# Kernel optimization log

Hardware: AMD Instinct MI355X
Metric: run time of the kernel (lower is better)

## Reference

```python
import jax, jax.numpy as jnp
import numpy as np

B, T, DM, H, D = 2, 4096, 1024, 16, 64
HD = H * D
PHASE_SCALE = 10.0


def _multiscale_phasors(num_heads, head_dim):
    # Deterministic multiscale frequencies: RoPE-like geometric spacing over
    # the feature dim, with a per-head octave scale (reconstruction of the
    # registered buffer `freqs` from generate_multiscale_phasors).
    d = np.arange(head_dim, dtype=np.float32) / head_dim
    base = 10000.0 ** (-d)                      # (D,)
    head_scale = 2.0 ** (-np.arange(num_heads, dtype=np.float32))  # (H,)
    return jnp.asarray(2.0 * np.pi * head_scale[:, None] * base[None, :],
                       dtype=jnp.float32)       # (H, D)


def setup_inputs() -> dict:
    key = jax.random.key(0)
    k0, k1, k2, k3 = jax.random.split(key, 4)
    x = jax.random.normal(k0, (B, T, DM), jnp.float32)
    Wk = jax.random.normal(k1, (DM, HD), jnp.float32) / np.float32(np.sqrt(DM))
    Wv = jax.random.normal(k2, (DM, HD), jnp.float32) / np.float32(np.sqrt(DM))
    Wo = jax.random.normal(k3, (HD, DM), jnp.float32) / np.float32(np.sqrt(HD))
    gate = jnp.full((H, 2), 0.5, jnp.float32)
    freqs = _multiscale_phasors(H, D)
    return {"x": x, "Wk": Wk, "Wv": Wv, "Wo": Wo, "gate": gate, "freqs": freqs}


def _holo_fused_step(v, binder, probe):
    # (cumsum(v * binder, dim=1) * probe).real / sqrt(1..T)
    mem = jnp.cumsum(v * binder, axis=1)                     # (B,T,H,D) complex64
    t = v.shape[1]
    scale = jnp.sqrt(jnp.arange(1, t + 1, dtype=jnp.float32))[None, :, None, None]
    return jnp.real(mem * probe) / scale                     # (B,T,H,D) float32


def reference(x, Wk, Wv, Wo, gate, freqs):
    Bb, Tt, _ = x.shape
    k_real = (x @ Wk).reshape(Bb, Tt, H, D)                  # (B,T,H,D)
    v = (x @ Wv).reshape(Bb, Tt, H, D).astype(jnp.complex64)
    k = jnp.exp(1j * (k_real * PHASE_SCALE))                 # unit phasors, q = k
    # Positional path: rotors = exp(i * t * freqs)
    t = jnp.arange(Tt, dtype=jnp.float32)
    rotors = jnp.exp(1j * (t[:, None, None] * freqs))[None]  # (1,T,H,D)
    out_pos = _holo_fused_step(v, rotors, jnp.conj(rotors))
    # Associative path: bind with conj of shifted keys, retrieve with q=k
    k_shifted = jnp.roll(k, 1, axis=1).at[:, 0].set(0.0)
    out_assoc = _holo_fused_step(v, jnp.conj(k_shifted), k)
    g_pos = gate[:, 0][None, None, :, None]
    g_assoc = gate[:, 1][None, None, :, None]
    out = out_pos * g_pos + out_assoc * g_assoc              # (B,T,H,D)
    return out.reshape(Bb, Tt, HD) @ Wo                      # dropout p=0 -> identity
```

## Files before the change

kernel.cpp:

```cpp
#include <hip/hip_runtime.h>


#define B_ 2
#define T_ 4096
#define DM_ 1024
#define H_ 16
#define D_ 64
#define M_ (B_*T_)
#define PHASE_SCALE 10.0f

typedef _Float16 f16;
typedef unsigned int u32;
typedef __attribute__((ext_vector_type(8))) _Float16 f16x8;
typedef __attribute__((ext_vector_type(4))) _Float16 f16x4;
typedef __attribute__((ext_vector_type(4))) float f32x4;


__global__ void k_cvt_f32_f16(const float* __restrict__ src, f16* __restrict__ dst, int n) {
  int i = blockIdx.x * blockDim.x + threadIdx.x;
  int idx = i * 4;
  if (idx < n) {
    float4 v = *reinterpret_cast<const float4*>(src + idx);
    f16x4 o;
    o[0] = (f16)v.x; o[1] = (f16)v.y; o[2] = (f16)v.z; o[3] = (f16)v.w;
    *reinterpret_cast<f16x4*>(dst + idx) = o;
  }
}

__global__ void k_transpose_cvt(const float* __restrict__ src, f16* __restrict__ dst) {
  __shared__ float tile[32][33];
  int bx = blockIdx.x;
  int by = blockIdx.y;
  int tx = threadIdx.x;
  int ty = threadIdx.y;
  #pragma unroll
  for (int r = 0; r < 32; r += 8)
    tile[ty + r][tx] = src[(size_t)(by * 32 + ty + r) * 1024 + bx * 32 + tx];
  __syncthreads();
  #pragma unroll
  for (int r = 0; r < 32; r += 8)
    dst[(size_t)(bx * 32 + ty + r) * 1024 + by * 32 + tx] = (f16)tile[tx][ty + r];
}


__device__ __forceinline__ void gl2lds16(const void* g, void* l) {
  __builtin_amdgcn_global_load_lds((const __attribute__((address_space(1))) u32*)g,
                                   (__attribute__((address_space(3))) u32*)l, 16, 0, 0);
}

__launch_bounds__(256)
__global__ void k_gemm_f16(const f16* __restrict__ A, const f16* __restrict__ Bt,
                           float* __restrict__ C, int N, int K) {
  __shared__ f16 lA[128][32];
  __shared__ f16 lB[128][32];
  const int tid  = threadIdx.x;
  const int lane = tid & 63;
  const int wid  = tid >> 6;
  const int wr   = wid >> 1, wc = wid & 1;
  const int m0   = blockIdx.x * 128;
  const int n0   = blockIdx.y * 128;
  const int row_l = tid >> 2;
  const int seg   = (tid & 3) * 8;
  const int lr    = lane & 15;
  const int kofs  = (lane >> 4) * 8;

  f32x4 acc[4][4] = {};

  const f16* ga = A  + (size_t)(m0 + row_l) * K + seg;
  const f16* gb = Bt + (size_t)(n0 + row_l) * K + seg;

  for (int k0 = 0; k0 < K; k0 += 32) {
    gl2lds16(ga + k0,                 &lA[row_l][seg]);
    gl2lds16(ga + (size_t)64 * K + k0, &lA[64 + row_l][seg]);
    gl2lds16(gb + k0,                 &lB[row_l][seg]);
    gl2lds16(gb + (size_t)64 * K + k0, &lB[64 + row_l][seg]);
    __syncthreads();
    f16x8 af[4], bf[4];
    #pragma unroll
    for (int i = 0; i < 4; ++i)
      af[i] = *(const f16x8*)(&lA[wr * 64 + i * 16 + lr][kofs]);
    #pragma unroll
    for (int j = 0; j < 4; ++j)
      bf[j] = *(const f16x8*)(&lB[wc * 64 + j * 16 + lr][kofs]);
    #pragma unroll
    for (int i = 0; i < 4; ++i)
      #pragma unroll
      for (int j = 0; j < 4; ++j)
        acc[i][j] = __builtin_amdgcn_mfma_f32_16x16x32_f16(af[i], bf[j], acc[i][j], 0, 0, 0);
    __syncthreads();
  }

  const int rb = (lane >> 4) * 4;
  #pragma unroll
  for (int i = 0; i < 4; ++i) {
    const int row = m0 + wr * 64 + i * 16 + rb;
    #pragma unroll
    for (int j = 0; j < 4; ++j) {
      const int col = n0 + wc * 64 + j * 16 + lr;
      #pragma unroll
      for (int r = 0; r < 4; ++r)
        C[(size_t)(row + r) * N + col] = acc[i][j][r];
    }
  }
}


__global__ void k_scan_part(const float* __restrict__ kv, const float* __restrict__ freqs,
                            float4* __restrict__ tot) {
  const int bid = blockIdx.x;
  const int cg = bid & 15;
  const int h  = (bid >> 4) & 15;
  const int b  = bid >> 8;
  const int w  = threadIdx.x >> 6;
  const int d  = threadIdx.x & 63;
  const int c  = cg * 4 + w;
  const int t0 = c * 64;
  const int base = h * 64 + d;
  const float f = freqs[base];

  float bc = 0.f, bs = 0.f;
  if (t0 > 0) {
    float krp = kv[(size_t)(b * T_ + t0 - 1) * 2048 + base];
    float th = PHASE_SCALE * krp;
    bs = __sinf(th); bc = __cosf(th);
  }
  float pr = 0.f, pi = 0.f, ar = 0.f, ai = 0.f;
  #pragma unroll 4
  for (int tt = 0; tt < 64; ++tt) {
    int t = t0 + tt;
    size_t row = (size_t)(b * T_ + t) * 2048;
    float v  = kv[row + 1024 + base];
    float kr = kv[row + base];
    double rrev = (double)t * (double)f * 0.15915494309189535;
    rrev -= floor(rrev);
    float ph = (float)rrev * 6.28318530717958647692f;
    float sp = __sinf(ph), cp = __cosf(ph);
    pr += v * cp; pi += v * sp;
    ar += v * bc; ai -= v * bs;
    float th = PHASE_SCALE * kr;
    bs = __sinf(th); bc = __cosf(th);
  }
  tot[((size_t)(c * 2 + b) * 16 + h) * 64 + d] = make_float4(pr, pi, ar, ai);
}

__global__ void k_scan_carry(const float4* __restrict__ tot, float4* __restrict__ carry) {
  const int h = blockIdx.x & 15;
  const int b = blockIdx.x >> 4;
  const int d = threadIdx.x;
  float pr = 0.f, pi = 0.f, ar = 0.f, ai = 0.f;
  for (int c = 0; c < 64; ++c) {
    size_t idx = ((size_t)(c * 2 + b) * 16 + h) * 64 + d;
    float4 tv = tot[idx];
    carry[idx] = make_float4(pr, pi, ar, ai);
    pr += tv.x; pi += tv.y; ar += tv.z; ai += tv.w;
  }
}

__global__ void k_scan_out(const float* __restrict__ kv, const float* __restrict__ freqs,
                           const float4* __restrict__ carry, const float* __restrict__ gate,
                           f16* __restrict__ y) {
  const int bid = blockIdx.x;
  const int cg = bid & 15;
  const int h  = (bid >> 4) & 15;
  const int b  = bid >> 8;
  const int w  = threadIdx.x >> 6;
  const int d  = threadIdx.x & 63;
  const int c  = cg * 4 + w;
  const int t0 = c * 64;
  const int base = h * 64 + d;
  const float f = freqs[base];
  const float gp = gate[2 * h], ga = gate[2 * h + 1];

  float4 cr = carry[((size_t)(c * 2 + b) * 16 + h) * 64 + d];
  float pr = cr.x, pi = cr.y, ar = cr.z, ai = cr.w;
  float bc = 0.f, bs = 0.f;
  if (t0 > 0) {
    float krp = kv[(size_t)(b * T_ + t0 - 1) * 2048 + base];
    float th = PHASE_SCALE * krp;
    bs = __sinf(th); bc = __cosf(th);
  }
  #pragma unroll 4
  for (int tt = 0; tt < 64; ++tt) {
    int t = t0 + tt;
    size_t row = (size_t)(b * T_ + t) * 2048;
    float v  = kv[row + 1024 + base];
    float kr = kv[row + base];
    double rrev = (double)t * (double)f * 0.15915494309189535;
    rrev -= floor(rrev);
    float ph = (float)rrev * 6.28318530717958647692f;
    float sp = __sinf(ph), cp = __cosf(ph);
    pr += v * cp; pi += v * sp;
    ar += v * bc; ai -= v * bs;
    float th = PHASE_SCALE * kr;
    bs = __sinf(th); bc = __cosf(th);
    float inv = rsqrtf((float)(t + 1));
    float op = (pr * cp + pi * sp) * inv;
    float oa = (ar * bc - ai * bs) * inv;
    y[(size_t)(b * T_ + t) * 1024 + base] = (f16)(gp * op + ga * oa);
  }
}


extern "C" void kernel_launch(void* const* d_in, const int* in_sizes, int n_in,
                              void* d_out, int out_size, void* d_ws, size_t ws_size,
                              hipStream_t stream) {
  const float* x     = (const float*)d_in[0];
  const float* Wk    = (const float*)d_in[1];
  const float* Wv    = (const float*)d_in[2];
  const float* Wo    = (const float*)d_in[3];
  const float* gate  = (const float*)d_in[4];
  const float* freqs = (const float*)d_in[5];
  float* out = (float*)d_out;

  char* ws = (char*)d_ws;
  size_t off = 0;
  auto alloc = [&](size_t bytes) { void* p = ws + off; off += (bytes + 255) & ~255ull; return p; };

  f16*    xh    = (f16*)   alloc((size_t)M_ * DM_ * sizeof(f16));
  f16*    Wkvt  = (f16*)   alloc((size_t)2048 * 1024 * sizeof(f16));
  f16*    Wot   = (f16*)   alloc((size_t)1024 * 1024 * sizeof(f16));
  float*  kvb   = (float*) alloc((size_t)M_ * 2048 * sizeof(float));
  float4* tot   = (float4*)alloc((size_t)64 * B_ * H_ * D_ * sizeof(float4));
  float4* carry = (float4*)alloc((size_t)64 * B_ * H_ * D_ * sizeof(float4));
  f16*    yh    = xh;

  hipLaunchKernelGGL(k_cvt_f32_f16, dim3((M_ * DM_ / 4 + 255) / 256), dim3(256), 0, stream,
                     x, xh, M_ * DM_);
  hipLaunchKernelGGL(k_transpose_cvt, dim3(32, 32), dim3(32, 8), 0, stream, Wk, Wkvt);
  hipLaunchKernelGGL(k_transpose_cvt, dim3(32, 32), dim3(32, 8), 0, stream, Wv, Wkvt + (size_t)1024 * 1024);
  hipLaunchKernelGGL(k_transpose_cvt, dim3(32, 32), dim3(32, 8), 0, stream, Wo, Wot);
  hipLaunchKernelGGL(k_gemm_f16, dim3(64, 16), dim3(256), 0, stream, xh, Wkvt, kvb, 2048, 1024);
  hipLaunchKernelGGL(k_scan_part,  dim3(512), dim3(256), 0, stream, kvb, freqs, tot);
  hipLaunchKernelGGL(k_scan_carry, dim3(32),  dim3(64),  0, stream, tot, carry);
  hipLaunchKernelGGL(k_scan_out,   dim3(512), dim3(256), 0, stream, kvb, freqs, carry, gate, yh);
  hipLaunchKernelGGL(k_gemm_f16, dim3(64, 8), dim3(256), 0, stream, yh, Wot, out, 1024, 1024);
}
```

Before: 218.5 us.

## Replace GEMM with 256x256 pipelined swizzled kernel and restructure scan with rotor recurrence

```diff
diff --git a/kernel.cpp b/kernel.cpp
--- a/kernel.cpp
+++ b/kernel.cpp
@@ -3,7 +3,6 @@
 
 #define B_ 2
 #define T_ 4096
-#define DM_ 1024
 #define H_ 16
 #define D_ 64
 #define M_ (B_*T_)
@@ -17,8 +16,7 @@
 
 
 __global__ void k_cvt_f32_f16(const float* __restrict__ src, f16* __restrict__ dst, int n) {
-  int i = blockIdx.x * blockDim.x + threadIdx.x;
-  int idx = i * 4;
+  int idx = (blockIdx.x * blockDim.x + threadIdx.x) * 4;
   if (idx < n) {
     float4 v = *reinterpret_cast<const float4*>(src + idx);
     f16x4 o;
@@ -29,10 +27,8 @@
 
 __global__ void k_transpose_cvt(const float* __restrict__ src, f16* __restrict__ dst) {
   __shared__ float tile[32][33];
-  int bx = blockIdx.x;
-  int by = blockIdx.y;
-  int tx = threadIdx.x;
-  int ty = threadIdx.y;
+  int bx = blockIdx.x, by = blockIdx.y;
+  int tx = threadIdx.x, ty = threadIdx.y;
   #pragma unroll
   for (int r = 0; r < 32; r += 8)
     tile[ty + r][tx] = src[(size_t)(by * 32 + ty + r) * 1024 + bx * 32 + tx];
@@ -43,102 +39,174 @@
 }
 
 
-__device__ __forceinline__ void gl2lds16(const void* g, void* l) {
+__device__ __forceinline__ void gl2lds16(const f16* g, char* l) {
   __builtin_amdgcn_global_load_lds((const __attribute__((address_space(1))) u32*)g,
                                    (__attribute__((address_space(3))) u32*)l, 16, 0, 0);
 }
 
-__launch_bounds__(256)
-__global__ void k_gemm_f16(const f16* __restrict__ A, const f16* __restrict__ Bt,
-                           float* __restrict__ C, int N, int K) {
-  __shared__ f16 lA[128][32];
-  __shared__ f16 lB[128][32];
+#define S_BAR() __builtin_amdgcn_s_barrier()
+#define WAIT_LGKM0() do { asm volatile("s_waitcnt lgkmcnt(0)" ::: "memory"); \
+                          __builtin_amdgcn_sched_barrier(0); } while (0)
+#define WAIT_VM(n) asm volatile("s_waitcnt vmcnt(" #n ")" ::: "memory")
+
+#define STAGE(gp, ldsoff, kkt) do { \
+  gl2lds16((gp) + (size_t)(kkt) * 64,               smem + (ldsoff) + tid * 16); \
+  gl2lds16((gp) + (size_t)(kkt) * 64 + 64 * 1024,   smem + (ldsoff) + 8192 + tid * 16); \
+} while (0)
+
+#define PHASE(AH, BH, READ_A, VMW, STG) do { \
+  if (READ_A) { \
+    _Pragma("unroll") for (int mi = 0; mi < 4; ++mi) \
+    _Pragma("unroll") for (int kk = 0; kk < 2; ++kk) \
+      aF[mi][kk] = *(const f16x8*)(smem + curbuf + (AH) * 16384 + offA[mi][kk]); \
+  } \
+  _Pragma("unroll") for (int nj = 0; nj < 2; ++nj) \
+  _Pragma("unroll") for (int kk = 0; kk < 2; ++kk) \
+    bF[nj][kk] = *(const f16x8*)(smem + curbuf + 32768 + (BH) * 16384 + offB[nj][kk]); \
+  STG; \
+  S_BAR(); \
+  WAIT_LGKM0(); \
+  __builtin_amdgcn_s_setprio(1); \
+  _Pragma("unroll") for (int mi = 0; mi < 4; ++mi) \
+  _Pragma("unroll") for (int nj = 0; nj < 2; ++nj) \
+  _Pragma("unroll") for (int kk = 0; kk < 2; ++kk) \
+    acc[(AH) * 2 + (BH)][mi][nj] = __builtin_amdgcn_mfma_f32_16x16x32_f16( \
+        aF[mi][kk], bF[nj][kk], acc[(AH) * 2 + (BH)][mi][nj], 0, 0, 0); \
+  __builtin_amdgcn_s_setprio(0); \
+  VMW; \
+  S_BAR(); \
+} while (0)
+
+__launch_bounds__(512, 1)
+__global__ void k_gemm8(const f16* __restrict__ A, const f16* __restrict__ Bt,
+                        float* __restrict__ C32, f16* __restrict__ C16) {
+  extern __shared__ char smem[];
   const int tid  = threadIdx.x;
   const int lane = tid & 63;
   const int wid  = tid >> 6;
-  const int wr   = wid >> 1, wc = wid & 1;
-  const int m0   = blockIdx.x * 128;
-  const int n0   = blockIdx.y * 128;
-  const int row_l = tid >> 2;
-  const int seg   = (tid & 3) * 8;
-  const int lr    = lane & 15;
-  const int kofs  = (lane >> 4) * 8;
-
-  f32x4 acc[4][4] = {};
-
-  const f16* ga = A  + (size_t)(m0 + row_l) * K + seg;
-  const f16* gb = Bt + (size_t)(n0 + row_l) * K + seg;
-
-  for (int k0 = 0; k0 < K; k0 += 32) {
-    gl2lds16(ga + k0,                 &lA[row_l][seg]);
-    gl2lds16(ga + (size_t)64 * K + k0, &lA[64 + row_l][seg]);
-    gl2lds16(gb + k0,                 &lB[row_l][seg]);
-    gl2lds16(gb + (size_t)64 * K + k0, &lB[64 + row_l][seg]);
-    __syncthreads();
-    f16x8 af[4], bf[4];
+  const int wr   = wid >> 2, wc = wid & 3;
+  const int lr   = lane & 15, hi = lane >> 4;
+  const int m0   = blockIdx.x * 256;
+  const int n0   = blockIdx.y * 256;
+
+  const int rsub = tid >> 3;
+  const int csw  = ((tid & 7) ^ (rsub & 7)) * 8;
+  const f16* gA0 = A  + (size_t)(m0 + rsub) * 1024 + csw;
+  const f16* gA1 = gA0 + (size_t)128 * 1024;
+  const f16* gB0 = Bt + (size_t)(n0 + rsub) * 1024 + csw;
+  const f16* gB1 = gB0 + (size_t)128 * 1024;
+
+  int offA[4][2], offB[2][2];
+  #pragma unroll
+  for (int mi = 0; mi < 4; ++mi)
     #pragma unroll
-    for (int i = 0; i < 4; ++i)
-      af[i] = *(const f16x8*)(&lA[wr * 64 + i * 16 + lr][kofs]);
+    for (int kk = 0; kk < 2; ++kk) {
+      int row = wr * 64 + mi * 16 + lr;
+      offA[mi][kk] = row * 128 + (((kk * 4 + hi) ^ (row & 7)) << 4);
+    }
+  #pragma unroll
+  for (int nj = 0; nj < 2; ++nj)
     #pragma unroll
-    for (int j = 0; j < 4; ++j)
-      bf[j] = *(const f16x8*)(&lB[wc * 64 + j * 16 + lr][kofs]);
+    for (int kk = 0; kk < 2; ++kk) {
+      int row = wc * 32 + nj * 16 + lr;
+      offB[nj][kk] = row * 128 + (((kk * 4 + hi) ^ (row & 7)) << 4);
+    }
+
+  f32x4 acc[4][4][2] = {};
+  f16x8 aF[4][2], bF[2][2];
+
+  STAGE(gA0, 0,     0);
+  STAGE(gB0, 32768, 0);
+  STAGE(gA1, 16384, 0);
+  STAGE(gA0, 65536, 1);
+  STAGE(gB1, 49152, 0);
+  STAGE(gB0, 98304, 1);
+  WAIT_VM(8);
+  S_BAR();
+
+  for (int kt = 0; kt < 14; ++kt) {
+    const int curbuf = (kt & 1) * 65536;
+    const int nxtbuf = curbuf ^ 65536;
+    PHASE(0, 0, 1, WAIT_VM(4),  STAGE(gA1, nxtbuf + 16384, kt + 1));
+    PHASE(0, 1, 0, WAIT_VM(10), STAGE(gA0, curbuf + 0,     kt + 2));
+    PHASE(1, 0, 1, (void)0,     STAGE(gB1, nxtbuf + 49152, kt + 1));
+    PHASE(1, 1, 0, WAIT_VM(8),  STAGE(gB0, curbuf + 32768, kt + 2));
+  }
+  {
+    const int curbuf = 0, nxtbuf = 65536;
+    PHASE(0, 0, 1, WAIT_VM(4), STAGE(gA1, nxtbuf + 16384, 15));
+    PHASE(0, 1, 0, WAIT_VM(8), (void)0);
+    PHASE(1, 0, 1, (void)0,    STAGE(gB1, nxtbuf + 49152, 15));
+    PHASE(1, 1, 0, WAIT_VM(4), (void)0);
+  }
+  {
+    const int curbuf = 65536;
+    PHASE(0, 0, 1, WAIT_VM(0), (void)0);
+    PHASE(0, 1, 0, (void)0,    (void)0);
+    PHASE(1, 0, 1, (void)0,    (void)0);
+    PHASE(1, 1, 0, (void)0,    (void)0);
+  }
+
+  const int rb = hi * 4;
+  #pragma unroll
+  for (int ah = 0; ah < 2; ++ah)
     #pragma unroll
-    for (int i = 0; i < 4; ++i)
+    for (int bh = 0; bh < 2; ++bh)
       #pragma unroll
-      for (int j = 0; j < 4; ++j)
-        acc[i][j] = __builtin_amdgcn_mfma_f32_16x16x32_f16(af[i], bf[j], acc[i][j], 0, 0, 0);
-    __syncthreads();
-  }
-
-  const int rb = (lane >> 4) * 4;
-  #pragma unroll
-  for (int i = 0; i < 4; ++i) {
-    const int row = m0 + wr * 64 + i * 16 + rb;
-    #pragma unroll
-    for (int j = 0; j < 4; ++j) {
-      const int col = n0 + wc * 64 + j * 16 + lr;
-      #pragma unroll
-      for (int r = 0; r < 4; ++r)
-        C[(size_t)(row + r) * N + col] = acc[i][j][r];
-    }
-  }
-}
-
-
-__global__ void k_scan_part(const float* __restrict__ kv, const float* __restrict__ freqs,
-                            float4* __restrict__ tot) {
+      for (int mi = 0; mi < 4; ++mi)
+        #pragma unroll
+        for (int nj = 0; nj < 2; ++nj) {
+          f32x4 a4 = acc[ah * 2 + bh][mi][nj];
+          const int row = m0 + ah * 128 + wr * 64 + mi * 16 + rb;
+          const int col = n0 + bh * 128 + wc * 32 + nj * 16 + lr;
+          if (col < 1024) {
+            #pragma unroll
+            for (int r = 0; r < 4; ++r)
+              C32[(size_t)(row + r) * 1024 + col] = a4[r];
+          } else {
+            #pragma unroll
+            for (int r = 0; r < 4; ++r)
+              C16[(size_t)(row + r) * 1024 + (col - 1024)] = (f16)a4[r];
+          }
+        }
+}
+
+
+__global__ void k_scan_part(const float* __restrict__ kf, const f16* __restrict__ vh,
+                            const float* __restrict__ freqs, float4* __restrict__ tot) {
   const int bid = blockIdx.x;
-  const int cg = bid & 15;
-  const int h  = (bid >> 4) & 15;
-  const int b  = bid >> 8;
+  const int cg = bid & 31;
+  const int h  = (bid >> 5) & 15;
+  const int b  = bid >> 9;
   const int w  = threadIdx.x >> 6;
   const int d  = threadIdx.x & 63;
   const int c  = cg * 4 + w;
-  const int t0 = c * 64;
-  const int base = h * 64 + d;
-  const float f = freqs[base];
+  const int t0 = c * 32;
+  const int col = h * 64 + d;
+  const float f = freqs[col];
 
   float bc = 0.f, bs = 0.f;
   if (t0 > 0) {
-    float krp = kv[(size_t)(b * T_ + t0 - 1) * 2048 + base];
-    float th = PHASE_SCALE * krp;
-    bs = __sinf(th); bc = __cosf(th);
-  }
+    float krp = kf[(size_t)(b * T_ + t0 - 1) * 1024 + col];
+    __sincosf(PHASE_SCALE * krp, &bs, &bc);
+  }
+  double rev = (double)t0 * (double)f * 0.15915494309189535;
+  rev -= floor(rev);
+  float ph = (float)rev * 6.28318530717958647692f;
+  float ri, rc; __sincosf(ph, &ri, &rc);
+  float sf, cf; __sincosf(f, &sf, &cf);
+
   float pr = 0.f, pi = 0.f, ar = 0.f, ai = 0.f;
-  #pragma unroll 4
-  for (int tt = 0; tt < 64; ++tt) {
-    int t = t0 + tt;
-    size_t row = (size_t)(b * T_ + t) * 2048;
-    float v  = kv[row + 1024 + base];
-    float kr = kv[row + base];
-    double rrev = (double)t * (double)f * 0.15915494309189535;
-    rrev -= floor(rrev);
-    float ph = (float)rrev * 6.28318530717958647692f;
-    float sp = __sinf(ph), cp = __cosf(ph);
-    pr += v * cp; pi += v * sp;
-    ar += v * bc; ai -= v * bs;
-    float th = PHASE_SCALE * kr;
-    bs = __sinf(th); bc = __cosf(th);
+  #pragma unroll 8
+  for (int tt = 0; tt < 32; ++tt) {
+    size_t row = (size_t)(b * T_ + t0 + tt) * 1024 + col;
+    float v  = (float)vh[row];
+    float kr = kf[row];
+    pr = fmaf(v, rc, pr); pi = fmaf(v, ri, pi);
+    ar = fmaf(v, bc, ar); ai = fmaf(-v, bs, ai);
+    __sincosf(PHASE_SCALE * kr, &bs, &bc);
+    float nrc = rc * cf - ri * sf;
+    ri = rc * sf + ri * cf; rc = nrc;
   }
   tot[((size_t)(c * 2 + b) * 16 + h) * 64 + d] = make_float4(pr, pi, ar, ai);
 }
@@ -148,7 +216,7 @@
   const int b = blockIdx.x >> 4;
   const int d = threadIdx.x;
   float pr = 0.f, pi = 0.f, ar = 0.f, ai = 0.f;
-  for (int c = 0; c < 64; ++c) {
+  for (int c = 0; c < 128; ++c) {
     size_t idx = ((size_t)(c * 2 + b) * 16 + h) * 64 + d;
     float4 tv = tot[idx];
     carry[idx] = make_float4(pr, pi, ar, ai);
@@ -156,47 +224,50 @@
   }
 }
 
-__global__ void k_scan_out(const float* __restrict__ kv, const float* __restrict__ freqs,
-                           const float4* __restrict__ carry, const float* __restrict__ gate,
-                           f16* __restrict__ y) {
+__global__ void k_scan_out(const float* __restrict__ kf, const f16* __restrict__ vh,
+                           const float* __restrict__ freqs, const float4* __restrict__ carry,
+                           const float* __restrict__ gate, f16* __restrict__ y) {
   const int bid = blockIdx.x;
-  const int cg = bid & 15;
-  const int h  = (bid >> 4) & 15;
-  const int b  = bid >> 8;
+  const int cg = bid & 31;
+  const int h  = (bid >> 5) & 15;
+  const int b  = bid >> 9;
   const int w  = threadIdx.x >> 6;
   const int d  = threadIdx.x & 63;
   const int c  = cg * 4 + w;
-  const int t0 = c * 64;
-  const int base = h * 64 + d;
-  const float f = freqs[base];
+  const int t0 = c * 32;
+  const int col = h * 64 + d;
+  const float f = freqs[col];
   const float gp = gate[2 * h], ga = gate[2 * h + 1];
 
   float4 cr = carry[((size_t)(c * 2 + b) * 16 + h) * 64 + d];
   float pr = cr.x, pi = cr.y, ar = cr.z, ai = cr.w;
   float bc = 0.f, bs = 0.f;
   if (t0 > 0) {
-    float krp = kv[(size_t)(b * T_ + t0 - 1) * 2048 + base];
-    float th = PHASE_SCALE * krp;
-    bs = __sinf(th); bc = __cosf(th);
-  }
-  #pragma unroll 4
-  for (int tt = 0; tt < 64; ++tt) {
+    float krp = kf[(size_t)(b * T_ + t0 - 1) * 1024 + col];
+    __sincosf(PHASE_SCALE * krp, &bs, &bc);
+  }
+  double rev = (double)t0 * (double)f * 0.15915494309189535;
+  rev -= floor(rev);
+  float ph = (float)rev * 6.28318530717958647692f;
+  float ri, rc; __sincosf(ph, &ri, &rc);
+  float sf, cf; __sincosf(f, &sf, &cf);
+
+  #pragma unroll 8
+  for (int tt = 0; tt < 32; ++tt) {
     int t = t0 + tt;
-    size_t row = (size_t)(b * T_ + t) * 2048;
-    float v  = kv[row + 1024 + base];
-    float kr = kv[row + base];
-    double rrev = (double)t * (double)f * 0.15915494309189535;
-    rrev -= floor(rrev);
-    float ph = (float)rrev * 6.28318530717958647692f;
-    float sp = __sinf(ph), cp = __cosf(ph);
-    pr += v * cp; pi += v * sp;
-    ar += v * bc; ai -= v * bs;
-    float th = PHASE_SCALE * kr;
-    bs = __sinf(th); bc = __cosf(th);
+    size_t row = (size_t)(b * T_ + t) * 1024 + col;
+    float v  = (float)vh[row];
+    float kr = kf[row];
+    pr = fmaf(v, rc, pr); pi = fmaf(v, ri, pi);
+    ar = fmaf(v, bc, ar); ai = fmaf(-v, bs, ai);
+    float kc, ks; __sincosf(PHASE_SCALE * kr, &ks, &kc);
     float inv = rsqrtf((float)(t + 1));
-    float op = (pr * cp + pi * sp) * inv;
-    float oa = (ar * bc - ai * bs) * inv;
-    y[(size_t)(b * T_ + t) * 1024 + base] = (f16)(gp * op + ga * oa);
+    float op = fmaf(pr, rc, pi * ri) * inv;
+    float oa = fmaf(ar, kc, -(ai * ks)) * inv;
+    y[row] = (f16)(gp * op + ga * oa);
+    bs = ks; bc = kc;
+    float nrc = rc * cf - ri * sf;
+    ri = rc * sf + ri * cf; rc = nrc;
   }
 }
 
@@ -216,22 +287,26 @@
   size_t off = 0;
   auto alloc = [&](size_t bytes) { void* p = ws + off; off += (bytes + 255) & ~255ull; return p; };
 
-  f16*    xh    = (f16*)   alloc((size_t)M_ * DM_ * sizeof(f16));
+  f16*    xh    = (f16*)   alloc((size_t)M_ * 1024 * sizeof(f16));
   f16*    Wkvt  = (f16*)   alloc((size_t)2048 * 1024 * sizeof(f16));
   f16*    Wot   = (f16*)   alloc((size_t)1024 * 1024 * sizeof(f16));
-  float*  kvb   = (float*) alloc((size_t)M_ * 2048 * sizeof(float));
-  float4* tot   = (float4*)alloc((size_t)64 * B_ * H_ * D_ * sizeof(float4));
-  float4* carry = (float4*)alloc((size_t)64 * B_ * H_ * D_ * sizeof(float4));
+  float*  kf    = (float*) alloc((size_t)M_ * 1024 * sizeof(float));
+  f16*    vh    = (f16*)   alloc((size_t)M_ * 1024 * sizeof(f16));
+  float4* tot   = (float4*)alloc((size_t)128 * B_ * H_ * D_ * sizeof(float4));
+  float4* carry = (float4*)alloc((size_t)128 * B_ * H_ * D_ * sizeof(float4));
   f16*    yh    = xh;
 
-  hipLaunchKernelGGL(k_cvt_f32_f16, dim3((M_ * DM_ / 4 + 255) / 256), dim3(256), 0, stream,
-                     x, xh, M_ * DM_);
+  hipFuncSetAttribute(reinterpret_cast<const void*>(&k_gemm8),
+                      hipFuncAttributeMaxDynamicSharedMemorySize, 131072);
+
+  hipLaunchKernelGGL(k_cvt_f32_f16, dim3((M_ * 1024 / 4 + 255) / 256), dim3(256), 0, stream,
+                     x, xh, M_ * 1024);
   hipLaunchKernelGGL(k_transpose_cvt, dim3(32, 32), dim3(32, 8), 0, stream, Wk, Wkvt);
   hipLaunchKernelGGL(k_transpose_cvt, dim3(32, 32), dim3(32, 8), 0, stream, Wv, Wkvt + (size_t)1024 * 1024);
   hipLaunchKernelGGL(k_transpose_cvt, dim3(32, 32), dim3(32, 8), 0, stream, Wo, Wot);
-  hipLaunchKernelGGL(k_gemm_f16, dim3(64, 16), dim3(256), 0, stream, xh, Wkvt, kvb, 2048, 1024);
-  hipLaunchKernelGGL(k_scan_part,  dim3(512), dim3(256), 0, stream, kvb, freqs, tot);
-  hipLaunchKernelGGL(k_scan_carry, dim3(32),  dim3(64),  0, stream, tot, carry);
-  hipLaunchKernelGGL(k_scan_out,   dim3(512), dim3(256), 0, stream, kvb, freqs, carry, gate, yh);
-  hipLaunchKernelGGL(k_gemm_f16, dim3(64, 8), dim3(256), 0, stream, yh, Wot, out, 1024, 1024);
-}
+  hipLaunchKernelGGL(k_gemm8, dim3(32, 8), dim3(512), 131072, stream, xh, Wkvt, kf, vh);
+  hipLaunchKernelGGL(k_scan_part,  dim3(1024), dim3(256), 0, stream, kf, vh, freqs, tot);
+  hipLaunchKernelGGL(k_scan_carry, dim3(32),   dim3(64),  0, stream, tot, carry);
+  hipLaunchKernelGGL(k_scan_out,   dim3(1024), dim3(256), 0, stream, kf, vh, freqs, carry, gate, yh);
+  hipLaunchKernelGGL(k_gemm8, dim3(32, 4), dim3(512), 131072, stream, yh, Wot, out, nullptr);
+}
```

Result: faster. 203.1 us (-7.1%).
